# Kernel tuning notes

Measured on AMD Instinct MI355X. Metric: run time of the kernel, lower is better.

The kernel has to match this reference:

```python
import jax, jax.numpy as jnp
import numpy as np

CHUNK = 128  # chunk size for the causal linear-attention recurrence
EPS = 1e-10


def _causal_numerator(q, k, v, chunk=CHUNK):
    """N_i = sum_{j<=i} (q_i . k_j) v_j, computed chunk-recurrently.

    q,k: [B,H,N,D]; v: [B,H,N,E] -> [B,H,N,E]
    """
    B, H, N, D = q.shape
    E = v.shape[-1]
    nc = N // chunk
    qc = jnp.moveaxis(q.reshape(B, H, nc, chunk, D), 2, 0)  # [nc,B,H,c,D]
    kc = jnp.moveaxis(k.reshape(B, H, nc, chunk, D), 2, 0)
    vc = jnp.moveaxis(v.reshape(B, H, nc, chunk, E), 2, 0)
    mask = jnp.tril(jnp.ones((chunk, chunk), dtype=q.dtype))  # causal within chunk

    def step(S, inp):  # S: running sum of k_j (outer) v_j -> [B,H,D,E]
        qi, ki, vi = inp
        scores = jnp.einsum('bhid,bhjd->bhij', qi, ki) * mask
        intra = jnp.einsum('bhij,bhje->bhie', scores, vi)
        inter = jnp.einsum('bhid,bhde->bhie', qi, S)
        S = S + jnp.einsum('bhjd,bhje->bhde', ki, vi)
        return S, intra + inter

    S0 = jnp.zeros((B, H, D, E), q.dtype)
    _, outs = jax.lax.scan(step, S0, (qc, kc, vc))  # [nc,B,H,c,E]
    return jnp.moveaxis(outs, 0, 2).reshape(B, H, N, E)


def _causal_denominator(q, k):
    # D_i = q_i . cumsum_j<=i k_j  -> [B,H,N]
    return jnp.einsum('bhnd,bhnd->bhn', q, jnp.cumsum(k, axis=-2))


def setup_inputs() -> dict:
    key = jax.random.key(0)
    ks = jax.random.split(key, 5)
    shape = (2, 8, 4096, 64)
    names = ['q', 'k', 'q_rot', 'k_rot', 'v']
    # feature-mapped inputs (Performer softmax features) are positive
    return {n: jax.random.uniform(ks[i], shape, dtype=jnp.float32) for i, n in enumerate(names)}


def reference(q, k, q_rot, k_rot, v):
    N = _causal_numerator(q, k, v) + _causal_numerator(q_rot, k_rot, v)
    D = _causal_denominator(q, k) + _causal_denominator(q_rot, k_rot)
    return N * (1.0 / (D + EPS))[..., None]
```

## Files before the change

### kernel.cpp

```cpp
#include <hip/hip_runtime.h>

#define SEQ 4096
#define DIM 64
#define CHUNK 128
#define NC 32
#define EPSV 1e-10f
#define KS_OFF 2097152

typedef __attribute__((ext_vector_type(8))) short s16x8;
typedef __attribute__((ext_vector_type(4))) float f32x4;

__device__ __forceinline__ unsigned short f2bf(float f) {
  unsigned int u = __float_as_uint(f);
  u += 0x7FFF + ((u >> 16) & 1);
  return (unsigned short)(u >> 16);
}
__device__ __forceinline__ float bf2f(unsigned short s) {
  return __uint_as_float(((unsigned int)s) << 16);
}
__device__ __forceinline__ s16x8 pack8(float4 a, float4 b) {
  s16x8 r;
  r[0] = (short)f2bf(a.x); r[1] = (short)f2bf(a.y); r[2] = (short)f2bf(a.z); r[3] = (short)f2bf(a.w);
  r[4] = (short)f2bf(b.x); r[5] = (short)f2bf(b.y); r[6] = (short)f2bf(b.z); r[7] = (short)f2bf(b.w);
  return r;
}

__device__ __forceinline__ void stage_nat(const float* __restrict__ gp,
                                          unsigned short* __restrict__ nat, int t) {
#pragma unroll
  for (int p = 0; p < 8; ++p) {
    int idx = t + p * 256;
    int i = idx >> 4, d4 = idx & 15;
    float4 x = ((const float4*)gp)[idx];
    ushort4 u = make_ushort4(f2bf(x.x), f2bf(x.y), f2bf(x.z), f2bf(x.w));
    *(ushort4*)&nat[i * 72 + d4 * 4] = u;
  }
}

__device__ __forceinline__ void transpose_to_T(const unsigned short* __restrict__ nat,
                                               unsigned short* __restrict__ dst, int t) {
  int L = t & 63, w = t >> 6;
#pragma unroll
  for (int it = 0; it < 4; ++it) {
    int d = L, j8 = it * 4 + w;
    s16x8 seg;
#pragma unroll
    for (int u = 0; u < 8; ++u) seg[u] = (short)nat[(j8 * 8 + u) * 72 + d];
    *(s16x8*)&dst[d * 136 + j8 * 8] = seg;
  }
}

__global__ __launch_bounds__(256) void pass_a(const float* __restrict__ k0,
                                              const float* __restrict__ k1,
                                              const float* __restrict__ v,
                                              float* __restrict__ ws) {
  __shared__ __align__(16) unsigned short skT[64 * 136];
  __shared__ __align__(16) unsigned short svT[64 * 136];
  __shared__ __align__(16) unsigned short snat[128 * 72];
  int bid = blockIdx.x;
  int m = bid >> 9, rem = bid & 511, hh = rem >> 5, c = rem & 31;
  const float* kp = (m ? k1 : k0) + (size_t)hh * SEQ * DIM + (size_t)c * CHUNK * DIM;
  const float* vp = v + (size_t)hh * SEQ * DIM + (size_t)c * CHUNK * DIM;
  int t = threadIdx.x;

  stage_nat(kp, snat, t);
  __syncthreads();
  transpose_to_T(snat, skT, t);
  __syncthreads();
  stage_nat(vp, snat, t);
  __syncthreads();
  transpose_to_T(snat, svT, t);
  __syncthreads();

  if (t < 64) {
    float s = 0.f;
    for (int it = 0; it < 16; ++it) {
      s16x8 blk = *(const s16x8*)&skT[t * 136 + it * 8];
#pragma unroll
      for (int u = 0; u < 8; ++u) s += bf2f((unsigned short)blk[u]);
    }
    ws[KS_OFF + (size_t)bid * 64 + t] = s;
  }

  int w = t >> 6, L = t & 63, g = L >> 4, cL = L & 15;
  f32x4 acc[4];
#pragma unroll
  for (int ct = 0; ct < 4; ++ct) acc[ct] = (f32x4){0.f, 0.f, 0.f, 0.f};
#pragma unroll
  for (int ks = 0; ks < 4; ++ks) {
    s16x8 aF = *(const s16x8*)&svT[(w * 16 + cL) * 136 + ks * 32 + g * 8];
#pragma unroll
    for (int ct = 0; ct < 4; ++ct) {
      s16x8 bF = *(const s16x8*)&skT[(ct * 16 + cL) * 136 + ks * 32 + g * 8];
      acc[ct] = __builtin_amdgcn_mfma_f32_16x16x32_bf16(aF, bF, acc[ct], 0, 0, 0);
    }
  }
  unsigned short* Sp = (unsigned short*)ws + (size_t)bid * 4096;
#pragma unroll
  for (int ct = 0; ct < 4; ++ct)
#pragma unroll
    for (int r = 0; r < 4; ++r)
      Sp[(size_t)(w * 16 + g * 4 + r) * 64 + ct * 16 + cL] = f2bf(acc[ct][r]);
}

__global__ __launch_bounds__(256) void pass_b(float* __restrict__ ws) {
  int t = threadIdx.x;
  if (blockIdx.x < 256) {
    int gid = blockIdx.x * 256 + t;
    int mh = gid >> 11, de2 = gid & 2047;
    unsigned int* p = (unsigned int*)ws + (size_t)mh * NC * 2048 + de2;
    unsigned int x[NC];
#pragma unroll
    for (int c = 0; c < NC; ++c) x[c] = p[(size_t)c * 2048];
    float r0 = 0.f, r1 = 0.f;
#pragma unroll
    for (int c = 0; c < NC; ++c) {
      unsigned int xc = x[c];
      p[(size_t)c * 2048] = (unsigned int)f2bf(r0) | ((unsigned int)f2bf(r1) << 16);
      r0 += bf2f((unsigned short)(xc & 0xFFFF));
      r1 += bf2f((unsigned short)(xc >> 16));
    }
  } else {
    int gid = (blockIdx.x - 256) * 256 + t;
    int mh = gid >> 6, d = gid & 63;
    float* p = ws + KS_OFF + (size_t)mh * NC * 64 + d;
    float x[NC];
#pragma unroll
    for (int c = 0; c < NC; ++c) x[c] = p[(size_t)c * 64];
    float run = 0.f;
#pragma unroll
    for (int c = 0; c < NC; ++c) {
      p[(size_t)c * 64] = run;
      run += x[c];
    }
  }
}

__global__ __launch_bounds__(256) void pass_c(const float* __restrict__ q0,
                                              const float* __restrict__ q1,
                                              const float* __restrict__ k0,
                                              const float* __restrict__ k1,
                                              const float* __restrict__ v,
                                              const float* __restrict__ ws,
                                              float* __restrict__ out) {
  __shared__ __align__(16) unsigned short svT[64 * 136];
  __shared__ __align__(16) unsigned short sun[128 * 72];
  __shared__ float skpref[64];
  __shared__ float sden[128];

  int hh = blockIdx.x >> 5, c = blockIdx.x & 31;
  int t = threadIdx.x;
  int w = t >> 6, L = t & 63, g = L >> 4, cL = L & 15;
  size_t off = (size_t)hh * SEQ * DIM + (size_t)c * CHUNK * DIM;
  int rt_of[2] = {w, 7 - w};

  stage_nat(v + off, sun, t);
  __syncthreads();
  transpose_to_T(sun, svT, t);

  f32x4 accO[2][4];
#pragma unroll
  for (int a = 0; a < 2; ++a)
#pragma unroll
    for (int b = 0; b < 4; ++b) accO[a][b] = (f32x4){0.f, 0.f, 0.f, 0.f};
  float denfrag[2][4] = {};
  float denp[2] = {0.f, 0.f};

  const unsigned short* Sbase = (const unsigned short*)ws;

  for (int m = 0; m < 2; ++m) {
    const float* qp = (m ? q1 : q0) + off;
    const float* kp = (m ? k1 : k0) + off;
    const unsigned short* Sp = Sbase + (size_t)(m * 512 + hh * 32 + c) * 4096;
    const float* Kp = ws + KS_OFF + (size_t)(m * 512 + hh * 32 + c) * 64;

    __syncthreads();
#pragma unroll
    for (int p2 = 0; p2 < 2; ++p2) {
      int idx = t + p2 * 256;
      int e = idx >> 3, seg = idx & 7;
      *(s16x8*)&sun[e * 72 + seg * 8] = *(const s16x8*)&Sp[idx * 8];
    }
    if (t < 64) skpref[t] = Kp[t];
    __syncthreads();

    float kpf[2][8];
#pragma unroll
    for (int h = 0; h < 2; ++h) {
      float4 c0 = *(const float4*)&skpref[h * 32 + g * 8];
      float4 c1 = *(const float4*)&skpref[h * 32 + g * 8 + 4];
      kpf[h][0] = c0.x; kpf[h][1] = c0.y; kpf[h][2] = c0.z; kpf[h][3] = c0.w;
      kpf[h][4] = c1.x; kpf[h][5] = c1.y; kpf[h][6] = c1.z; kpf[h][7] = c1.w;
    }

    s16x8 aq[2][2];
#pragma unroll
    for (int ti = 0; ti < 2; ++ti) {
      int row = rt_of[ti] * 16 + cL;
#pragma unroll
      for (int h = 0; h < 2; ++h) {
        const float* qa = qp + row * 64 + h * 32 + g * 8;
        float4 a0 = *(const float4*)qa;
        float4 a1 = *(const float4*)(qa + 4);
        denp[ti] += a0.x * kpf[h][0] + a0.y * kpf[h][1] + a0.z * kpf[h][2] + a0.w * kpf[h][3]
                  + a1.x * kpf[h][4] + a1.y * kpf[h][5] + a1.z * kpf[h][6] + a1.w * kpf[h][7];
        aq[ti][h] = pack8(a0, a1);
      }
    }

#pragma unroll
    for (int h = 0; h < 2; ++h) {
#pragma unroll
      for (int et = 0; et < 4; ++et) {
        s16x8 bS = *(const s16x8*)&sun[(et * 16 + cL) * 72 + h * 32 + g * 8];
        accO[0][et] = __builtin_amdgcn_mfma_f32_16x16x32_bf16(aq[0][h], bS, accO[0][et], 0, 0, 0);
        accO[1][et] = __builtin_amdgcn_mfma_f32_16x16x32_bf16(aq[1][h], bS, accO[1][et], 0, 0, 0);
      }
    }
    __syncthreads();

    for (int s = 0; s <= (7 - w) >> 1; ++s) {
      s16x8 bK[2][2];
#pragma unroll
      for (int ct01 = 0; ct01 < 2; ++ct01) {
        int jrow = (2 * s + ct01) * 16 + cL;
#pragma unroll
        for (int h = 0; h < 2; ++h) {
          const float* ka = kp + jrow * 64 + h * 32 + g * 8;
          float4 b0 = *(const float4*)ka;
          float4 b1 = *(const float4*)(ka + 4);
          bK[ct01][h] = pack8(b0, b1);
        }
      }
#pragma unroll
      for (int ti = 0; ti < 2; ++ti) {
        int rt = rt_of[ti];
        if (2 * s > rt) continue;
        int rowbase = rt * 16 + g * 4;
#pragma unroll
        for (int ct01 = 0; ct01 < 2; ++ct01) {
          int jt = 2 * s + ct01;
          if (jt > rt) {
#pragma unroll
            for (int r = 0; r < 4; ++r) sun[(rowbase + r) * 40 + ct01 * 16 + cL] = 0;
          } else {
            f32x4 C = (f32x4){0.f, 0.f, 0.f, 0.f};
            C = __builtin_amdgcn_mfma_f32_16x16x32_bf16(aq[ti][0], bK[ct01][0], C, 0, 0, 0);
            C = __builtin_amdgcn_mfma_f32_16x16x32_bf16(aq[ti][1], bK[ct01][1], C, 0, 0, 0);
            if (jt == rt) {
#pragma unroll
              for (int r = 0; r < 4; ++r)
                if (cL > g * 4 + r) C[r] = 0.f;
            }
#pragma unroll
            for (int r = 0; r < 4; ++r) {
              denfrag[ti][r] += C[r];
              sun[(rowbase + r) * 40 + ct01 * 16 + cL] = f2bf(C[r]);
            }
          }
        }
      }
      asm volatile("s_waitcnt lgkmcnt(0)" ::: "memory");

      s16x8 bV[4];
#pragma unroll
      for (int et = 0; et < 4; ++et)
        bV[et] = *(const s16x8*)&svT[(et * 16 + cL) * 136 + s * 32 + g * 8];
#pragma unroll
      for (int ti = 0; ti < 2; ++ti) {
        if (2 * s > rt_of[ti]) continue;
        s16x8 aP = *(const s16x8*)&sun[(rt_of[ti] * 16 + cL) * 40 + g * 8];
#pragma unroll
        for (int et = 0; et < 4; ++et)
          accO[ti][et] = __builtin_amdgcn_mfma_f32_16x16x32_bf16(aP, bV[et], accO[ti][et], 0, 0, 0);
      }
    }
  }

#pragma unroll
  for (int ti = 0; ti < 2; ++ti) {
    denp[ti] += __shfl_xor(denp[ti], 16);
    denp[ti] += __shfl_xor(denp[ti], 32);
  }
  if (L < 16) {
    sden[rt_of[0] * 16 + L] = denp[0];
    sden[rt_of[1] * 16 + L] = denp[1];
  }
  __syncthreads();

  float* op = out + off;
#pragma unroll
  for (int ti = 0; ti < 2; ++ti) {
#pragma unroll
    for (int r = 0; r < 4; ++r) {
      float vs = denfrag[ti][r];
      vs += __shfl_xor(vs, 1);
      vs += __shfl_xor(vs, 2);
      vs += __shfl_xor(vs, 4);
      vs += __shfl_xor(vs, 8);
      int row = rt_of[ti] * 16 + g * 4 + r;
      float inv = 1.f / (sden[row] + vs + EPSV);
#pragma unroll
      for (int et = 0; et < 4; ++et)
        op[(size_t)row * 64 + et * 16 + cL] = accO[ti][et][r] * inv;
    }
  }
}

extern "C" void kernel_launch(void* const* d_in, const int* in_sizes, int n_in,
                              void* d_out, int out_size, void* d_ws, size_t ws_size,
                              hipStream_t stream) {
  const float* q  = (const float*)d_in[0];
  const float* k  = (const float*)d_in[1];
  const float* qr = (const float*)d_in[2];
  const float* kr = (const float*)d_in[3];
  const float* v  = (const float*)d_in[4];
  float* out = (float*)d_out;
  float* ws  = (float*)d_ws;

  hipLaunchKernelGGL(pass_a, dim3(1024), dim3(256), 0, stream, k, kr, v, ws);
  hipLaunchKernelGGL(pass_b, dim3(264), dim3(256), 0, stream, ws);
  hipLaunchKernelGGL(pass_c, dim3(512), dim3(256), 0, stream, q, qr, k, kr, v, ws, out);
}
```

Before: 140.9 us.

## Gather-transpose from global directly, prefetch K tiles, full-row P buffer in pass_c

Replaces the two-step stage-then-transpose through shared memory with a direct strided global gather into the transposed bf16 layout. This removes several barriers and a staging buffer, and the key column sum now comes from fp32 values instead of bf16. In pass_c the Q loads are hoisted ahead of the barrier and each K tile is prefetched into registers one step ahead. The full intra-chunk score matrix is written to a larger P buffer in LDS so the score*V MFMAs run as one pass after the score loop, rather than interleaved per pair of tiles. This trades more LDS and registers for fewer syncs and better latency hiding, with possible lower occupancy and uncoalesced strided global reads.

New measurement: 137.9 us. 2.1% less time.

```diff
diff --git a/kernel.cpp b/kernel.cpp
--- a/kernel.cpp
+++ b/kernel.cpp
@@ -15,9 +15,6 @@
   u += 0x7FFF + ((u >> 16) & 1);
   return (unsigned short)(u >> 16);
 }
-__device__ __forceinline__ float bf2f(unsigned short s) {
-  return __uint_as_float(((unsigned int)s) << 16);
-}
 __device__ __forceinline__ s16x8 pack8(float4 a, float4 b) {
   s16x8 r;
   r[0] = (short)f2bf(a.x); r[1] = (short)f2bf(a.y); r[2] = (short)f2bf(a.z); r[3] = (short)f2bf(a.w);
@@ -25,29 +22,28 @@
   return r;
 }
 
-__device__ __forceinline__ void stage_nat(const float* __restrict__ gp,
-                                          unsigned short* __restrict__ nat, int t) {
-#pragma unroll
-  for (int p = 0; p < 8; ++p) {
-    int idx = t + p * 256;
-    int i = idx >> 4, d4 = idx & 15;
-    float4 x = ((const float4*)gp)[idx];
-    ushort4 u = make_ushort4(f2bf(x.x), f2bf(x.y), f2bf(x.z), f2bf(x.w));
-    *(ushort4*)&nat[i * 72 + d4 * 4] = u;
-  }
-}
-
-__device__ __forceinline__ void transpose_to_T(const unsigned short* __restrict__ nat,
-                                               unsigned short* __restrict__ dst, int t) {
-  int L = t & 63, w = t >> 6;
-#pragma unroll
-  for (int it = 0; it < 4; ++it) {
-    int d = L, j8 = it * 4 + w;
+template<bool SUM>
+__device__ __forceinline__ float gather_T(const float* __restrict__ gp,
+                                          unsigned short* __restrict__ dst, int t) {
+  int d = t & 63, w6 = t >> 6;
+  float s = 0.f;
+#pragma unroll
+  for (int i = 0; i < 4; ++i) {
+    int j8 = w6 + i * 4;
+    const float* p = gp + (size_t)(j8 * 8) * DIM + d;
+    float x[8];
+#pragma unroll
+    for (int u = 0; u < 8; ++u) x[u] = p[(size_t)u * DIM];
+    if (SUM) {
+#pragma unroll
+      for (int u = 0; u < 8; ++u) s += x[u];
+    }
     s16x8 seg;
 #pragma unroll
-    for (int u = 0; u < 8; ++u) seg[u] = (short)nat[(j8 * 8 + u) * 72 + d];
+    for (int u = 0; u < 8; ++u) seg[u] = (short)f2bf(x[u]);
     *(s16x8*)&dst[d * 136 + j8 * 8] = seg;
   }
+  return s;
 }
 
 __global__ __launch_bounds__(256) void pass_a(const float* __restrict__ k0,
@@ -56,31 +52,20 @@
                                               float* __restrict__ ws) {
   __shared__ __align__(16) unsigned short skT[64 * 136];
   __shared__ __align__(16) unsigned short svT[64 * 136];
-  __shared__ __align__(16) unsigned short snat[128 * 72];
+  __shared__ float spart[4][64];
   int bid = blockIdx.x;
   int m = bid >> 9, rem = bid & 511, hh = rem >> 5, c = rem & 31;
   const float* kp = (m ? k1 : k0) + (size_t)hh * SEQ * DIM + (size_t)c * CHUNK * DIM;
   const float* vp = v + (size_t)hh * SEQ * DIM + (size_t)c * CHUNK * DIM;
   int t = threadIdx.x;
 
-  stage_nat(kp, snat, t);
+  float s = gather_T<true>(kp, skT, t);
+  gather_T<false>(vp, svT, t);
+  spart[t >> 6][t & 63] = s;
   __syncthreads();
-  transpose_to_T(snat, skT, t);
-  __syncthreads();
-  stage_nat(vp, snat, t);
-  __syncthreads();
-  transpose_to_T(snat, svT, t);
-  __syncthreads();
-
-  if (t < 64) {
-    float s = 0.f;
-    for (int it = 0; it < 16; ++it) {
-      s16x8 blk = *(const s16x8*)&skT[t * 136 + it * 8];
-#pragma unroll
-      for (int u = 0; u < 8; ++u) s += bf2f((unsigned short)blk[u]);
-    }
-    ws[KS_OFF + (size_t)bid * 64 + t] = s;
-  }
+
+  if (t < 64)
+    ws[KS_OFF + (size_t)bid * 64 + t] = spart[0][t] + spart[1][t] + spart[2][t] + spart[3][t];
 
   int w = t >> 6, L = t & 63, g = L >> 4, cL = L & 15;
   f32x4 acc[4];
@@ -117,8 +102,8 @@
     for (int c = 0; c < NC; ++c) {
       unsigned int xc = x[c];
       p[(size_t)c * 2048] = (unsigned int)f2bf(r0) | ((unsigned int)f2bf(r1) << 16);
-      r0 += bf2f((unsigned short)(xc & 0xFFFF));
-      r1 += bf2f((unsigned short)(xc >> 16));
+      r0 += __uint_as_float((xc & 0xFFFFu) << 16);
+      r1 += __uint_as_float(xc & 0xFFFF0000u);
     }
   } else {
     int gid = (blockIdx.x - 256) * 256 + t;
@@ -144,7 +129,8 @@
                                               const float* __restrict__ ws,
                                               float* __restrict__ out) {
   __shared__ __align__(16) unsigned short svT[64 * 136];
-  __shared__ __align__(16) unsigned short sun[128 * 72];
+  __shared__ __align__(16) unsigned short sST[64 * 72];
+  __shared__ __align__(16) unsigned short sP[128 * 136];
   __shared__ float skpref[64];
   __shared__ float sden[128];
 
@@ -152,11 +138,9 @@
   int t = threadIdx.x;
   int w = t >> 6, L = t & 63, g = L >> 4, cL = L & 15;
   size_t off = (size_t)hh * SEQ * DIM + (size_t)c * CHUNK * DIM;
-  int rt_of[2] = {w, 7 - w};
-
-  stage_nat(v + off, sun, t);
-  __syncthreads();
-  transpose_to_T(sun, svT, t);
+  int rt0 = w, rt1 = 7 - w;
+
+  gather_T<false>(v + off, svT, t);
 
   f32x4 accO[2][4];
 #pragma unroll
@@ -168,18 +152,31 @@
 
   const unsigned short* Sbase = (const unsigned short*)ws;
 
+#pragma unroll
   for (int m = 0; m < 2; ++m) {
     const float* qp = (m ? q1 : q0) + off;
     const float* kp = (m ? k1 : k0) + off;
     const unsigned short* Sp = Sbase + (size_t)(m * 512 + hh * 32 + c) * 4096;
     const float* Kp = ws + KS_OFF + (size_t)(m * 512 + hh * 32 + c) * 64;
 
-    __syncthreads();
+    float4 qa0[2][2], qa1[2][2];
+#pragma unroll
+    for (int ti = 0; ti < 2; ++ti) {
+      int row = (ti ? rt1 : rt0) * 16 + cL;
+#pragma unroll
+      for (int h = 0; h < 2; ++h) {
+        const float* qb = qp + (size_t)row * DIM + h * 32 + g * 8;
+        qa0[ti][h] = *(const float4*)qb;
+        qa1[ti][h] = *(const float4*)(qb + 4);
+      }
+    }
+
+    if (m) __syncthreads();
+
 #pragma unroll
     for (int p2 = 0; p2 < 2; ++p2) {
       int idx = t + p2 * 256;
-      int e = idx >> 3, seg = idx & 7;
-      *(s16x8*)&sun[e * 72 + seg * 8] = *(const s16x8*)&Sp[idx * 8];
+      *(s16x8*)&sST[(idx >> 3) * 72 + (idx & 7) * 8] = *(const s16x8*)&Sp[idx * 8];
     }
     if (t < 64) skpref[t] = Kp[t];
     __syncthreads();
@@ -195,81 +192,86 @@
 
     s16x8 aq[2][2];
 #pragma unroll
-    for (int ti = 0; ti < 2; ++ti) {
-      int row = rt_of[ti] * 16 + cL;
+    for (int ti = 0; ti < 2; ++ti)
 #pragma unroll
       for (int h = 0; h < 2; ++h) {
-        const float* qa = qp + row * 64 + h * 32 + g * 8;
-        float4 a0 = *(const float4*)qa;
-        float4 a1 = *(const float4*)(qa + 4);
+        float4 a0 = qa0[ti][h], a1 = qa1[ti][h];
         denp[ti] += a0.x * kpf[h][0] + a0.y * kpf[h][1] + a0.z * kpf[h][2] + a0.w * kpf[h][3]
                   + a1.x * kpf[h][4] + a1.y * kpf[h][5] + a1.z * kpf[h][6] + a1.w * kpf[h][7];
         aq[ti][h] = pack8(a0, a1);
       }
-    }
-
-#pragma unroll
-    for (int h = 0; h < 2; ++h) {
+
+#pragma unroll
+    for (int h = 0; h < 2; ++h)
 #pragma unroll
       for (int et = 0; et < 4; ++et) {
-        s16x8 bS = *(const s16x8*)&sun[(et * 16 + cL) * 72 + h * 32 + g * 8];
+        s16x8 bS = *(const s16x8*)&sST[(et * 16 + cL) * 72 + h * 32 + g * 8];
         accO[0][et] = __builtin_amdgcn_mfma_f32_16x16x32_bf16(aq[0][h], bS, accO[0][et], 0, 0, 0);
         accO[1][et] = __builtin_amdgcn_mfma_f32_16x16x32_bf16(aq[1][h], bS, accO[1][et], 0, 0, 0);
       }
-    }
-    __syncthreads();
-
-    for (int s = 0; s <= (7 - w) >> 1; ++s) {
-      s16x8 bK[2][2];
-#pragma unroll
-      for (int ct01 = 0; ct01 < 2; ++ct01) {
-        int jrow = (2 * s + ct01) * 16 + cL;
+
+    float4 kc0[2], kc1[2];
+    {
+      const float* kb = kp + (size_t)cL * DIM;
+#pragma unroll
+      for (int h = 0; h < 2; ++h) {
+        kc0[h] = *(const float4*)(kb + h * 32 + g * 8);
+        kc1[h] = *(const float4*)(kb + h * 32 + g * 8 + 4);
+      }
+    }
+    for (int jt = 0; jt <= rt1; ++jt) {
+      float4 kn0[2], kn1[2];
+      if (jt < rt1) {
+        const float* kb = kp + (size_t)((jt + 1) * 16 + cL) * DIM;
 #pragma unroll
         for (int h = 0; h < 2; ++h) {
-          const float* ka = kp + jrow * 64 + h * 32 + g * 8;
-          float4 b0 = *(const float4*)ka;
-          float4 b1 = *(const float4*)(ka + 4);
-          bK[ct01][h] = pack8(b0, b1);
+          kn0[h] = *(const float4*)(kb + h * 32 + g * 8);
+          kn1[h] = *(const float4*)(kb + h * 32 + g * 8 + 4);
         }
       }
+      s16x8 bK0 = pack8(kc0[0], kc1[0]);
+      s16x8 bK1 = pack8(kc0[1], kc1[1]);
 #pragma unroll
       for (int ti = 0; ti < 2; ++ti) {
-        int rt = rt_of[ti];
-        if (2 * s > rt) continue;
-        int rowbase = rt * 16 + g * 4;
-#pragma unroll
-        for (int ct01 = 0; ct01 < 2; ++ct01) {
-          int jt = 2 * s + ct01;
-          if (jt > rt) {
-#pragma unroll
-            for (int r = 0; r < 4; ++r) sun[(rowbase + r) * 40 + ct01 * 16 + cL] = 0;
-          } else {
-            f32x4 C = (f32x4){0.f, 0.f, 0.f, 0.f};
-            C = __builtin_amdgcn_mfma_f32_16x16x32_bf16(aq[ti][0], bK[ct01][0], C, 0, 0, 0);
-            C = __builtin_amdgcn_mfma_f32_16x16x32_bf16(aq[ti][1], bK[ct01][1], C, 0, 0, 0);
-            if (jt == rt) {
-#pragma unroll
-              for (int r = 0; r < 4; ++r)
-                if (cL > g * 4 + r) C[r] = 0.f;
-            }
-#pragma unroll
-            for (int r = 0; r < 4; ++r) {
-              denfrag[ti][r] += C[r];
-              sun[(rowbase + r) * 40 + ct01 * 16 + cL] = f2bf(C[r]);
-            }
-          }
+        int rt = ti ? rt1 : rt0;
+        if (jt > rt) continue;
+        f32x4 C = (f32x4){0.f, 0.f, 0.f, 0.f};
+        C = __builtin_amdgcn_mfma_f32_16x16x32_bf16(aq[ti][0], bK0, C, 0, 0, 0);
+        C = __builtin_amdgcn_mfma_f32_16x16x32_bf16(aq[ti][1], bK1, C, 0, 0, 0);
+        if (jt == rt) {
+#pragma unroll
+          for (int r = 0; r < 4; ++r)
+            if (cL > g * 4 + r) C[r] = 0.f;
         }
-      }
-      asm volatile("s_waitcnt lgkmcnt(0)" ::: "memory");
-
+#pragma unroll
+        for (int r = 0; r < 4; ++r) {
+          denfrag[ti][r] += C[r];
+          sP[(size_t)(rt * 16 + g * 4 + r) * 136 + jt * 16 + cL] = f2bf(C[r]);
+        }
+      }
+#pragma unroll
+      for (int h = 0; h < 2; ++h) { kc0[h] = kn0[h]; kc1[h] = kn1[h]; }
+    }
+    {
+      int rte = (rt0 & 1) ? rt1 : rt0;
+#pragma unroll
+      for (int r = 0; r < 4; ++r)
+        sP[(size_t)(rte * 16 + g * 4 + r) * 136 + (rte + 1) * 16 + cL] = 0;
+    }
+
+    asm volatile("s_waitcnt lgkmcnt(0)" ::: "memory");
+
+#pragma unroll
+    for (int ks = 0; ks < 4; ++ks) {
       s16x8 bV[4];
 #pragma unroll
       for (int et = 0; et < 4; ++et)
-        bV[et] = *(const s16x8*)&svT[(et * 16 + cL) * 136 + s * 32 + g * 8];
+        bV[et] = *(const s16x8*)&svT[(et * 16 + cL) * 136 + ks * 32 + g * 8];
 #pragma unroll
       for (int ti = 0; ti < 2; ++ti) {
-        if (2 * s > rt_of[ti]) continue;
-        s16x8 aP = *(const s16x8*)&sun[(rt_of[ti] * 16 + cL) * 40 + g * 8];
+        int rt = ti ? rt1 : rt0;
+        if (ks > (rt >> 1)) continue;
+        s16x8 aP = *(const s16x8*)&sP[(size_t)(rt * 16 + cL) * 136 + ks * 32 + g * 8];
 #pragma unroll
         for (int et = 0; et < 4; ++et)
           accO[ti][et] = __builtin_amdgcn_mfma_f32_16x16x32_bf16(aP, bV[et], accO[ti][et], 0, 0, 0);
@@ -283,14 +285,15 @@
     denp[ti] += __shfl_xor(denp[ti], 32);
   }
   if (L < 16) {
-    sden[rt_of[0] * 16 + L] = denp[0];
-    sden[rt_of[1] * 16 + L] = denp[1];
+    sden[rt0 * 16 + L] = denp[0];
+    sden[rt1 * 16 + L] = denp[1];
   }
   __syncthreads();
 
   float* op = out + off;
 #pragma unroll
   for (int ti = 0; ti < 2; ++ti) {
+    int rt = ti ? rt1 : rt0;
 #pragma unroll
     for (int r = 0; r < 4; ++r) {
       float vs = denfrag[ti][r];
@@ -298,7 +301,7 @@
       vs += __shfl_xor(vs, 2);
       vs += __shfl_xor(vs, 4);
       vs += __shfl_xor(vs, 8);
-      int row = rt_of[ti] * 16 + g * 4 + r;
+      int row = rt * 16 + g * 4 + r;
       float inv = 1.f / (sden[row] + vs + EPSV);
 #pragma unroll
       for (int et = 0; et < 4; ++et)
```
